# Optimization experiments

Hardware: AMD Instinct MI355X
Metric: run time of the kernel (lower is better)

The kernel has to match this reference:

```python
import jax, jax.numpy as jnp
import numpy as np

B, N = 4, 65536
NUM_GROUP, GROUP_SIZE = 512, 64
EMB = 60


def setup_inputs() -> dict:
    key = jax.random.key(0)
    ks = jax.random.split(key, 8)
    inp = {
        'xyz': jax.random.uniform(ks[0], (B, N, 3), jnp.float32),
        'color': jax.random.uniform(ks[1], (B, N, 3), jnp.float32),
        'W1': jax.random.normal(ks[2], (6, 64), jnp.float32) * 0.2,
        'b1': jnp.zeros((64,), jnp.float32),
        'W2': jax.random.normal(ks[3], (64, 128), jnp.float32) * 0.1,
        'b2': jnp.zeros((128,), jnp.float32),
        'W3': jax.random.normal(ks[4], (128, 256), jnp.float32) * 0.08,
        'b3': jnp.zeros((256,), jnp.float32),
        'W4': jax.random.normal(ks[5], (256, 512), jnp.float32) * 0.06,
        'b4': jnp.zeros((512,), jnp.float32),
        'Wp': jax.random.normal(ks[6], (512, EMB), jnp.float32) * 0.04,
        'bp': jnp.zeros((EMB,), jnp.float32),
    }
    return inp


def fps(xyz, n):
    """Farthest point sampling. xyz: (B,N,3) -> centers (B,n,3)."""
    b, npts, _ = xyz.shape
    start = jnp.zeros((b,), jnp.int32)
    d0 = jnp.full((b, npts), 1e10, xyz.dtype)

    def step(carry, _):
        dists, last = carry
        p = jnp.take_along_axis(xyz, last[:, None, None], axis=1)  # (B,1,3)
        d = jnp.sum((xyz - p) ** 2, axis=-1)                       # (B,N)
        dists = jnp.minimum(dists, d)
        nxt = jnp.argmax(dists, axis=-1).astype(jnp.int32)
        return (dists, nxt), nxt

    (_, _), rest = jax.lax.scan(step, (d0, start), None, length=n - 1)
    idx = jnp.concatenate([start[:, None], rest.T], axis=1)        # (B,n)
    return jax.vmap(lambda pts, i: pts[i])(xyz, idx)


def knn_idx(k, xyz, new_xyz):
    """Indices of k nearest points in xyz for each query in new_xyz.
    xyz: (B,N,3), new_xyz: (B,S,3) -> (B,S,k) int32. Matches
    square_distance + topk(largest=False)."""
    sq = (jnp.sum(new_xyz ** 2, -1)[..., None]
          + jnp.sum(xyz ** 2, -1)[:, None, :]
          - 2.0 * jnp.einsum('bsc,bnc->bsn', new_xyz, xyz))        # (B,S,N)
    _, idx = jax.lax.top_k(-sq, k)
    return idx


def reference(xyz, color, W1, b1, W2, b2, W3, b3, W4, b4, Wp, bp):
    # --- Group: FPS centers + KNN neighborhood gather + centering ---
    center = fps(xyz, NUM_GROUP)                                   # (B,G,3)
    idx = knn_idx(GROUP_SIZE, xyz, center)                         # (B,G,M)
    gather = jax.vmap(lambda pts, i: pts[i])                       # pts[(B,)N,3], i (G,M)
    neighborhood = gather(xyz, idx) - center[:, :, None, :]        # (B,G,M,3) centered
    neighborhood_color = gather(color, idx)                        # (B,G,M,3)
    feats = jnp.concatenate([neighborhood, neighborhood_color], -1)  # (B,G,M,6)

    # --- PointNet: per-point MLP -> max over group -> projection ---
    x = jax.nn.relu(feats @ W1 + b1)
    x = jax.nn.relu(x @ W2 + b2)
    x = jax.nn.relu(x @ W3 + b3)
    x = jax.nn.relu(x @ W4 + b4)                                   # (B,G,M,512)
    x = jnp.max(x, axis=2)                                         # (B,G,512)
    emb = x @ Wp + bp                                              # (B,G,60)
    return emb, center
```

## Files before the change

### kernel.cpp

```cpp
#include <hip/hip_runtime.h>
#include <stdint.h>

#define DI __device__ __forceinline__

typedef _Float16 f16x8 __attribute__((ext_vector_type(8)));
typedef float f32x4 __attribute__((ext_vector_type(4)));
typedef unsigned long long u64;
typedef unsigned short u16;

constexpr int kB = 4;
constexpr int kN = 65536;
constexpr int kG = 512;
constexpr int kM = 64;
constexpr int kE = 60;
constexpr int GRD = 16;
constexpr int NCELL = GRD * GRD * GRD;
constexpr int NSUP = 512;
constexpr float CW = 1.0f / 16.0f;

constexpr int TPB = 512;
constexpr int NWORK = 252;
constexpr int NBLK = 256;

constexpr size_t OFF_CLINE  = 0;
constexpr size_t OFF_CCNT   = OFF_CLINE + (size_t)kB * kG * 128;
constexpr size_t OFF_GS     = OFF_CCNT + (size_t)kB * NCELL * 4;
constexpr size_t ZERO_BYTES = OFF_GS + 64;
constexpr size_t OFF_CSTART = (ZERO_BYTES + 255) & ~(size_t)255;
constexpr size_t OFF_CUR    = OFF_CSTART + (size_t)kB * (NCELL + 1) * 4;
constexpr size_t OFF_DD     = ((OFF_CUR + (size_t)kB * NCELL * 4) + 255) & ~(size_t)255;
constexpr size_t OFF_SW1    = (OFF_DD + (size_t)kB * kN * 4 + 255) & ~(size_t)255;
constexpr size_t OFF_SW2    = OFF_SW1 + 2048 * 2;
constexpr size_t OFF_SW3    = OFF_SW2 + 8192 * 2;
constexpr size_t OFF_SW4    = OFF_SW3 + 32768 * 2;
constexpr size_t OFF_WPT    = OFF_SW4 + 131072 * 2;
constexpr size_t OFF_SORT   = ((OFF_WPT + 60 * 512 * 4) + 255) & ~(size_t)255;

DI int cellof(float x) {
  int c = (int)(x * (float)GRD);
  return min(GRD - 1, max(0, c));
}
DI unsigned orderable(float f) {
  unsigned u = __float_as_uint(f);
  return (u & 0x80000000u) ? ~u : (u | 0x80000000u);
}

__global__ void k_zero(uint32_t* p, int nwords) {
  int i = blockIdx.x * blockDim.x + threadIdx.x;
  int st = gridDim.x * blockDim.x;
  for (; i < nwords; i += st) p[i] = 0u;
}

DI void swz(const float* __restrict__ W, _Float16* __restrict__ sw,
            int total, int nks, int Kreal, int N, int i0, int st) {
  for (int i = i0; i < total; i += st) {
    int j = i & 7, lane = (i >> 3) & 63, rest = i >> 9;
    int ks = rest % nks, nt = rest / nks;
    int k = ks * 32 + ((lane >> 4) << 3) + j;
    int n = nt * 16 + (lane & 15);
    sw[i] = (_Float16)((k < Kreal) ? W[k * N + n] : 0.f);
  }
}

__global__ void k_prep(const float* __restrict__ W1, const float* __restrict__ W2,
                       const float* __restrict__ W3, const float* __restrict__ W4,
                       const float* __restrict__ Wp,
                       _Float16* __restrict__ sw1, _Float16* __restrict__ sw2,
                       _Float16* __restrict__ sw3, _Float16* __restrict__ sw4,
                       float* __restrict__ wpt) {
  int i0 = blockIdx.x * blockDim.x + threadIdx.x;
  int st = gridDim.x * blockDim.x;
  swz(W1, sw1, 2048, 1, 6, 64, i0, st);
  swz(W2, sw2, 8192, 2, 64, 128, i0, st);
  swz(W3, sw3, 32768, 4, 128, 256, i0, st);
  swz(W4, sw4, 131072, 8, 256, 512, i0, st);
  for (int i = i0; i < 60 * 512; i += st) { int n = i >> 9, k = i & 511; wpt[i] = Wp[k * 60 + n]; }
}

DI void gbar(uint32_t* ctr, unsigned target) {
  __syncthreads();
  if (threadIdx.x == 0) {
    __hip_atomic_fetch_add(ctr, 1u, __ATOMIC_ACQ_REL, __HIP_MEMORY_SCOPE_AGENT);
    long bail = 0;
    while (__hip_atomic_load(ctr, __ATOMIC_ACQUIRE, __HIP_MEMORY_SCOPE_AGENT) < target) {
      __builtin_amdgcn_s_sleep(32);
      if (++bail > 100000000L) break;
    }
  }
  __syncthreads();
}

template <bool FIRST>
DI u64 refine_cell(int c, const float4* __restrict__ SP, float* __restrict__ DD,
                   const uint32_t* __restrict__ lcs,
                   float cx, float cy, float cz, int lig) {
  int s0 = (int)lcs[c], s1 = (int)lcs[c + 1];
  int pbase = s0 + lig;
  float4 pt[8];
  float ddo[8];
#pragma unroll
  for (int j = 0; j < 8; ++j) {
    int p = pbase + 4 * j;
    int pc = max(min(p, s1 - 1), 0);
    pt[j] = SP[pc];
    ddo[j] = FIRST ? 1e10f : DD[pc];
  }
  u64 key = 0ull;
#pragma unroll
  for (int j = 0; j < 8; ++j) {
    int p = pbase + 4 * j;
    if (p < s1) {
      float dx = __fsub_rn(pt[j].x, cx);
      float dy = __fsub_rn(pt[j].y, cy);
      float dz = __fsub_rn(pt[j].z, cz);
      float d = __fadd_rn(__fadd_rn(__fmul_rn(dx, dx), __fmul_rn(dy, dy)), __fmul_rn(dz, dz));
      float nd = fminf(ddo[j], d);
      DD[p] = nd;
      u64 k = ((u64)__float_as_uint(nd) << 32) |
              (u64)(0xFFFFFFFFu - (unsigned)__float_as_uint(pt[j].w));
      key = (k > key) ? k : key;
    }
  }
  for (int p = pbase + 32; p < s1; p += 4) {
    float4 pp = SP[p];
    float od = FIRST ? 1e10f : DD[p];
    float dx = __fsub_rn(pp.x, cx);
    float dy = __fsub_rn(pp.y, cy);
    float dz = __fsub_rn(pp.z, cz);
    float d = __fadd_rn(__fadd_rn(__fmul_rn(dx, dx), __fmul_rn(dy, dy)), __fmul_rn(dz, dz));
    float nd = fminf(od, d);
    DD[p] = nd;
    u64 k = ((u64)__float_as_uint(nd) << 32) |
            (u64)(0xFFFFFFFFu - (unsigned)__float_as_uint(pp.w));
    key = (k > key) ? k : key;
  }
  u64 o = __shfl_xor(key, 1); key = (o > key) ? o : key;
  o = __shfl_xor(key, 2); key = (o > key) ? o : key;
  return key;
}

DI void fps_block(const float* __restrict__ xyz, float* __restrict__ outC,
                  u64* __restrict__ cline, uint32_t* __restrict__ gs,
                  const float4* __restrict__ sorted_g,
                  const uint32_t* __restrict__ cstart_g,
                  float* __restrict__ dd_g, int b, char* smem) {
  __builtin_amdgcn_s_setprio(3);
  const int tid = threadIdx.x;
  const int wv = tid >> 6, lane = tid & 63;
  const int grp4 = tid >> 2, lig = tid & 3;
  const float* X = xyz + (size_t)b * kN * 3;
  const float4* SP = sorted_g + (size_t)b * kN;
  float* DD = dd_g + (size_t)b * kN;
  u64* cl = cline + (size_t)b * kG * 16;

  u64* ckey = (u64*)smem;
  uint32_t* lcs = (uint32_t*)(smem + 32768);
  u16* queue = (u16*)(smem + 49408);
  u16* squeue = (u16*)(smem + 57600);
  uint32_t* skey32 = (uint32_t*)(smem + 58624);
  int* qn = (int*)(smem + 60672);
  int* qsn = (int*)(smem + 60676);
  u64* warr = (u64*)(smem + 60736);
  float4* wbuf = (float4*)(smem + 60800);

  float cx = X[0], cy = X[1], cz = X[2];
  if (tid == 0) {
    u64 tg = 1u;
    __hip_atomic_store(cl + 0, ((u64)__float_as_uint(cx) << 32) | tg, __ATOMIC_RELAXED, __HIP_MEMORY_SCOPE_AGENT);
    __hip_atomic_store(cl + 1, ((u64)__float_as_uint(cy) << 32) | tg, __ATOMIC_RELAXED, __HIP_MEMORY_SCOPE_AGENT);
    __hip_atomic_store(cl + 2, ((u64)__float_as_uint(cz) << 32) | tg, __ATOMIC_RELAXED, __HIP_MEMORY_SCOPE_AGENT);
    outC[(size_t)b * kG * 3 + 0] = cx;
    outC[(size_t)b * kG * 3 + 1] = cy;
    outC[(size_t)b * kG * 3 + 2] = cz;
    long bail = 0;
    while (__hip_atomic_load(gs + 2, __ATOMIC_ACQUIRE, __HIP_MEMORY_SCOPE_AGENT) < NWORK) {
      __builtin_amdgcn_s_sleep(16);
      if (++bail > 200000000L) break;
    }
    *qn = 0; *qsn = 0;
  }
  __syncthreads();
  for (int i = tid; i <= NCELL; i += TPB) lcs[i] = cstart_g[(size_t)b * (NCELL + 1) + i];
  __syncthreads();

  for (int it = 1; it < kG; ++it) {
    if (it > 1) {
      {
        int s = tid;
        int sx = s & 7, sy = (s >> 3) & 7, sz = s >> 6;
        float x0 = (float)sx * (2.f * CW);
        float y0 = (float)sy * (2.f * CW);
        float z0 = (float)sz * (2.f * CW);
        float dx = fmaxf(fmaxf(x0 - cx, cx - (x0 + 2.f * CW)), 0.f);
        float dy = fmaxf(fmaxf(y0 - cy, cy - (y0 + 2.f * CW)), 0.f);
        float dz = fmaxf(fmaxf(z0 - cz, cz - (z0 + 2.f * CW)), 0.f);
        float lb = dx * dx + dy * dy + dz * dz;
        bool need = !(lb * 0.999f > __uint_as_float(skey32[s]));
        u64 m = __ballot(need);
        int base = 0;
        if (lane == 0) base = atomicAdd(qsn, (int)__popcll(m));
        base = __shfl(base, 0);
        if (need) squeue[base + (int)__popcll(m & ((1ull << lane) - 1ull))] = (u16)s;
      }
      __syncthreads();
      {
        const int Qs = *qsn;
        int g8 = lane >> 3, lig8 = lane & 7;
        for (int t0 = 0; t0 < Qs; t0 += 64) {
          int t = t0 + wv * 8 + g8;
          bool act = t < Qs;
          int ss = act ? (int)squeue[t] : 0;
          int sx = ss & 7, sy = (ss >> 3) & 7, sz = ss >> 6;
          int cxi = 2 * sx + (lig8 & 1);
          int cyi = 2 * sy + ((lig8 >> 1) & 1);
          int czi = 2 * sz + (lig8 >> 2);
          int c = (czi * GRD + cyi) * GRD + cxi;
          float x0 = (float)cxi * CW, y0 = (float)cyi * CW, z0 = (float)czi * CW;
          float dx = fmaxf(fmaxf(x0 - cx, cx - (x0 + CW)), 0.f);
          float dy = fmaxf(fmaxf(y0 - cy, cy - (y0 + CW)), 0.f);
          float dz = fmaxf(fmaxf(z0 - cz, cz - (z0 + CW)), 0.f);
          float lb = dx * dx + dy * dy + dz * dz;
          float ub = __uint_as_float(((const uint32_t*)ckey)[2 * c + 1]);
          bool need = act && !(lb * 0.999f > ub);
          u64 m = __ballot(need);
          int base = 0;
          if (lane == 0) base = atomicAdd(qn, (int)__popcll(m));
          base = __shfl(base, 0);
          if (need) queue[base + (int)__popcll(m & ((1ull << lane) - 1ull))] = (u16)c;
        }
      }
    }
    __syncthreads();
    if (it == 1) {
      for (int c = grp4; c < NCELL; c += 128) {
        u64 key = refine_cell<true>(c, SP, DD, lcs, cx, cy, cz, lig);
        if (lig == 0) ckey[c] = key;
      }
    } else {
      const int Q = *qn;
      for (int t = grp4; t < Q; t += 128) {
        int c = (int)queue[t];
        u64 key = refine_cell<false>(c, SP, DD, lcs, cx, cy, cz, lig);
        if (lig == 0) ckey[c] = key;
      }
    }
    __syncthreads();
    {
      int s = tid;
      int sx = s & 7, sy = (s >> 3) & 7, sz = s >> 6;
      u64 smax = 0ull;
#pragma unroll
      for (int d = 0; d < 8; ++d) {
        int cxi = 2 * sx + (d & 1);
        int cyi = 2 * sy + ((d >> 1) & 1);
        int czi = 2 * sz + (d >> 2);
        u64 k = ckey[(czi * GRD + cyi) * GRD + cxi];
        smax = (k > smax) ? k : smax;
      }
      skey32[s] = (uint32_t)(smax >> 32);
      u64 key = smax;
#pragma unroll
      for (int off = 32; off; off >>= 1) {
        u64 o = __shfl_xor(key, off);
        key = (o > key) ? o : key;
      }
      if (lane == 0) warr[wv] = key;
    }
    __syncthreads();
    if (tid == 0) {
      u64 k = warr[0];
#pragma unroll
      for (int i = 1; i < 8; ++i) k = (warr[i] > k) ? warr[i] : k;
      unsigned wi = 0xFFFFFFFFu - (unsigned)(k & 0xFFFFFFFFu);
      wbuf[it & 3] = make_float4(X[3 * wi], X[3 * wi + 1], X[3 * wi + 2], 0.f);
      *qn = 0; *qsn = 0;
    }
    __syncthreads();
    float4 wc = wbuf[it & 3];
    cx = wc.x; cy = wc.y; cz = wc.z;
    if ((it & 3) == 3 || it == kG - 1) {
      int k0 = it & ~3;
      if (tid <= (it & 3) && (k0 + tid) >= 1) {
        int itp = k0 + tid;
        float4 w = wbuf[tid];
        u64 tg = (unsigned)(itp + 1);
        u64* e = cl + (size_t)itp * 16;
        __hip_atomic_store(e + 0, ((u64)__float_as_uint(w.x) << 32) | tg, __ATOMIC_RELAXED, __HIP_MEMORY_SCOPE_AGENT);
        __hip_atomic_store(e + 1, ((u64)__float_as_uint(w.y) << 32) | tg, __ATOMIC_RELAXED, __HIP_MEMORY_SCOPE_AGENT);
        __hip_atomic_store(e + 2, ((u64)__float_as_uint(w.z) << 32) | tg, __ATOMIC_RELAXED, __HIP_MEMORY_SCOPE_AGENT);
        outC[((size_t)b * kG + itp) * 3 + 0] = w.x;
        outC[((size_t)b * kG + itp) * 3 + 1] = w.y;
        outC[((size_t)b * kG + itp) * 3 + 2] = w.z;
      }
    }
  }
}

DI void bitonic(u64* a, int n, int tid) {
  for (int k = 2; k <= n; k <<= 1)
    for (int j = k >> 1; j > 0; j >>= 1) {
      __syncthreads();
      for (int i = tid; i < n; i += TPB) {
        int ix = i ^ j;
        if (ix > i) {
          u64 x = a[i], y = a[ix];
          bool up = ((i & k) == 0);
          if ((x > y) == up) { a[i] = y; a[ix] = x; }
        }
      }
    }
  __syncthreads();
}

template <int Kdim, int Ndim, int SIN, int SOUT>
DI void mfma_layer(const _Float16* __restrict__ Xin, _Float16* __restrict__ Xout,
                   const _Float16* __restrict__ Wsw, const float* __restrict__ bias,
                   int wave, int lane) {
  constexpr int NKS = Kdim / 32;
  constexpr int NTW = Ndim / 64;
  constexpr int CH = (NTW < 4) ? NTW : 4;
  const int quad = lane >> 4, l16 = lane & 15;
  for (int c0 = 0; c0 < NTW; c0 += CH) {
    f32x4 acc[CH][4];
#pragma unroll
    for (int nt = 0; nt < CH; ++nt) {
      float bv = bias[wave * (Ndim / 4) + (c0 + nt) * 16 + l16];
#pragma unroll
      for (int m = 0; m < 4; ++m) acc[nt][m] = {bv, bv, bv, bv};
    }
#pragma unroll
    for (int ks = 0; ks < NKS; ++ks) {
      f16x8 af[4];
#pragma unroll
      for (int m = 0; m < 4; ++m)
        af[m] = *(const f16x8*)(Xin + (m * 16 + l16) * SIN + ks * 32 + quad * 8);
#pragma unroll
      for (int nt = 0; nt < CH; ++nt) {
        int ntg = wave * NTW + c0 + nt;
        f16x8 bf = *(const f16x8*)(Wsw + ((size_t)(ntg * NKS + ks) * 64 + lane) * 8);
#pragma unroll
        for (int m = 0; m < 4; ++m)
          acc[nt][m] = __builtin_amdgcn_mfma_f32_16x16x32_f16(af[m], bf, acc[nt][m], 0, 0, 0);
      }
    }
#pragma unroll
    for (int nt = 0; nt < CH; ++nt) {
      int col = wave * (Ndim / 4) + (c0 + nt) * 16 + l16;
#pragma unroll
      for (int m = 0; m < 4; ++m)
#pragma unroll
        for (int r = 0; r < 4; ++r) {
          int row = m * 16 + quad * 4 + r;
          Xout[row * SOUT + col] = (_Float16)fmaxf(acc[nt][m][r], 0.f);
        }
    }
  }
}

DI void mfma_layer4(const _Float16* __restrict__ Xin, const _Float16* __restrict__ Wsw,
                    const float* __restrict__ bias, float* __restrict__ maxv,
                    int wave, int lane) {
  constexpr int SIN = 264, NKS = 8, NTW = 8, CH = 4;
  const int quad = lane >> 4, l16 = lane & 15;
  for (int c0 = 0; c0 < NTW; c0 += CH) {
    f32x4 acc[CH][4];
#pragma unroll
    for (int nt = 0; nt < CH; ++nt) {
      float bv = bias[wave * 128 + (c0 + nt) * 16 + l16];
#pragma unroll
      for (int m = 0; m < 4; ++m) acc[nt][m] = {bv, bv, bv, bv};
    }
#pragma unroll
    for (int ks = 0; ks < NKS; ++ks) {
      f16x8 af[4];
#pragma unroll
      for (int m = 0; m < 4; ++m)
        af[m] = *(const f16x8*)(Xin + (m * 16 + l16) * SIN + ks * 32 + quad * 8);
#pragma unroll
      for (int nt = 0; nt < CH; ++nt) {
        int ntg = wave * NTW + c0 + nt;
        f16x8 bf = *(const f16x8*)(Wsw + ((size_t)(ntg * NKS + ks) * 64 + lane) * 8);
#pragma unroll
        for (int m = 0; m < 4; ++m)
          acc[nt][m] = __builtin_amdgcn_mfma_f32_16x16x32_f16(af[m], bf, acc[nt][m], 0, 0, 0);
      }
    }
#pragma unroll
    for (int nt = 0; nt < CH; ++nt) {
      float mx = 0.f;
#pragma unroll
      for (int m = 0; m < 4; ++m)
#pragma unroll
        for (int r = 0; r < 4; ++r) mx = fmaxf(mx, acc[nt][m][r]);
      mx = fmaxf(mx, __shfl_xor(mx, 16, 64));
      mx = fmaxf(mx, __shfl_xor(mx, 32, 64));
      if (quad == 0) maxv[wave * 128 + (c0 + nt) * 16 + l16] = mx;
    }
  }
}

__global__ __launch_bounds__(TPB, 2) void k_fused(
    const float* __restrict__ xyz, const float* __restrict__ color,
    float* __restrict__ outC, float* __restrict__ outE,
    u64* __restrict__ cline, uint32_t* __restrict__ ccnt,
    uint32_t* __restrict__ cstart, uint32_t* __restrict__ cur,
    float4* __restrict__ sorted, float* __restrict__ dd_g,
    uint32_t* __restrict__ gs,
    const _Float16* __restrict__ sw1, const _Float16* __restrict__ sw2,
    const _Float16* __restrict__ sw3, const _Float16* __restrict__ sw4,
    const float* __restrict__ wpt,
    const float* __restrict__ b1, const float* __restrict__ b2,
    const float* __restrict__ b3, const float* __restrict__ b4,
    const float* __restrict__ bp) {
  __shared__ __align__(16) char smem[65536];
  const int bi = blockIdx.x;
  if (bi < kB) {
    fps_block(xyz, outC, cline, gs, sorted, cstart, dd_g, bi, smem);
    return;
  }

  const int wj = bi - kB;
  const int tid = threadIdx.x;
  const int wave = tid >> 6, lane = tid & 63;
  __shared__ int nC;
  __shared__ float4 spc;
  __shared__ uint32_t s_part[TPB];
  u64* cand = (u64*)smem;

  for (int i = wj * TPB + tid; i < kB * kN; i += NWORK * TPB) {
    int b = i >> 16, p = i & (kN - 1);
    const float* q = xyz + ((size_t)b * kN + p) * 3;
    int cid = (cellof(q[2]) * GRD + cellof(q[1])) * GRD + cellof(q[0]);
    atomicAdd(&ccnt[b * NCELL + cid], 1u);
  }
  gbar(gs + 0, NWORK);
  if (wj < kB) {
    int b = wj;
    const uint32_t* cc = ccnt + (size_t)b * NCELL;
    uint32_t* cs = cstart + (size_t)b * (NCELL + 1);
    uint32_t* cu = cur + (size_t)b * NCELL;
    const int chunk = NCELL / TPB;
    int c0 = tid * chunk;
    uint32_t s = 0;
    for (int i = 0; i < chunk; ++i) s += cc[c0 + i];
    s_part[tid] = s;
    __syncthreads();
    for (int off = 1; off < TPB; off <<= 1) {
      uint32_t add = (tid >= off) ? s_part[tid - off] : 0u;
      __syncthreads();
      s_part[tid] += add;
      __syncthreads();
    }
    uint32_t run = s_part[tid] - s;
    for (int i = 0; i < chunk; ++i) {
      int c = c0 + i;
      cs[c] = run; cu[c] = run; run += cc[c];
    }
    if (tid == TPB - 1) cs[NCELL] = run;
  }
  gbar(gs + 1, NWORK);
  for (int i = wj * TPB + tid; i < kB * kN; i += NWORK * TPB) {
    int b = i >> 16, p = i & (kN - 1);
    const float* q = xyz + ((size_t)b * kN + p) * 3;
    float x = q[0], y = q[1], z = q[2];
    int cid = (cellof(z) * GRD + cellof(y)) * GRD + cellof(x);
    uint32_t pos = atomicAdd(&cur[b * NCELL + cid], 1u);
    sorted[(size_t)b * kN + pos] = make_float4(x, y, z, __uint_as_float((unsigned)p));
  }
  gbar(gs + 2, NWORK);

  for (int j = wj; j < kB * kG; j += NWORK) {
    const int it = j >> 2, b = j & 3;
    if (tid < 64) {
      const u64* e = cline + ((size_t)b * kG + it) * 16;
      u64 v = 0; long bail = 0;
      for (;;) {
        if (lane < 3)
          v = __hip_atomic_load(e + lane, __ATOMIC_RELAXED, __HIP_MEMORY_SCOPE_AGENT);
        bool ok = (lane >= 3) || ((unsigned)v == (unsigned)(it + 1));
        if (__all(ok)) break;
        __builtin_amdgcn_s_sleep(8);
        if (++bail > 100000000L) break;
      }
      u64 v0 = __shfl(v, 0), v1 = __shfl(v, 1), v2 = __shfl(v, 2);
      if (tid == 0)
        spc = make_float4(__uint_as_float((unsigned)(v0 >> 32)),
                          __uint_as_float((unsigned)(v1 >> 32)),
                          __uint_as_float((unsigned)(v2 >> 32)), 0.f);
    }
    __syncthreads();
    const float cx = spc.x, cy = spc.y, cz = spc.z;

    const float nc = __fadd_rn(__fadd_rn(__fmul_rn(cx, cx), __fmul_rn(cy, cy)), __fmul_rn(cz, cz));
    const float4* SPb = sorted + (size_t)b * kN;
    const uint32_t* CS = cstart + (size_t)b * (NCELL + 1);
    const int ccx = cellof(cx), ccy = cellof(cy), ccz = cellof(cz);
    if (tid == 0) nC = 0;
    __syncthreads();
    int plox = 1, phix = 0, ploy = 1, phiy = 0, ploz = 1, phiz = 0;
    for (int r = 1; r <= GRD; ++r) {
      int lox = max(0, ccx - r), hix = min(GRD - 1, ccx + r);
      int loy = max(0, ccy - r), hiy = min(GRD - 1, ccy + r);
      int loz = max(0, ccz - r), hiz = min(GRD - 1, ccz + r);
      for (int z = loz; z <= hiz; ++z)
        for (int y = loy; y <= hiy; ++y) {
          bool rowPrev = (r > 1) && (z >= ploz && z <= phiz && y >= ploy && y <= phiy);
          for (int s = 0; s < 2; ++s) {
            int xa, xb;
            if (!rowPrev) { if (s) break; xa = lox; xb = hix; }
            else if (s == 0) { xa = lox; xb = plox - 1; }
            else { xa = phix + 1; xb = hix; }
            if (xa > xb) continue;
            int c0 = (z * GRD + y) * GRD + xa;
            int i0 = CS[c0];
            int i1 = CS[(z * GRD + y) * GRD + xb + 1];
            for (int i = i0 + tid; i < i1; i += TPB) {
              float4 pt = SPb[i];
              float npn = __fadd_rn(__fadd_rn(__fmul_rn(pt.x, pt.x), __fmul_rn(pt.y, pt.y)),
                                    __fmul_rn(pt.z, pt.z));
              float dot = __fadd_rn(__fadd_rn(__fmul_rn(cx, pt.x), __fmul_rn(cy, pt.y)),
                                    __fmul_rn(cz, pt.z));
              float sq = __fsub_rn(__fadd_rn(nc, npn), __fmul_rn(2.0f, dot));
              unsigned key = orderable(sq);
              int pos = atomicAdd(&nC, 1);
              if (pos < 8192)
                cand[pos] = ((u64)key << 32) | (unsigned)__float_as_uint(pt.w);
            }
          }
        }
      __syncthreads();
      int n = min(nC, 8192);
      float rc = 1e30f;
      if (lox > 0) rc = fminf(rc, cx - (float)lox * CW);
      if (hix < GRD - 1) rc = fminf(rc, (float)(hix + 1) * CW - cx);
      if (loy > 0) rc = fminf(rc, cy - (float)loy * CW);
      if (hiy < GRD - 1) rc = fminf(rc, (float)(hiy + 1) * CW - cy);
      if (loz > 0) rc = fminf(rc, cz - (float)loz * CW);
      if (hiz < GRD - 1) rc = fminf(rc, (float)(hiz + 1) * CW - cz);
      float r2 = (rc >= 1e29f) ? 3.0e38f : rc * rc * (1.0f - 1e-5f);
      unsigned keyR = orderable(r2);
      bool done = false;
      if (n >= kM) {
        int np2 = 1;
        while (np2 < n) np2 <<= 1;
        for (int i = n + tid; i < np2; i += TPB) cand[i] = ~0ull;
        bitonic(cand, np2, tid);
        unsigned k63 = (unsigned)(cand[kM - 1] >> 32);
        done = (k63 <= keyR);
        if (tid == 0) nC = n;
      }
      __syncthreads();
      if (done) break;
      plox = lox; phix = hix; ploy = loy; phiy = hiy; ploz = loz; phiz = hiz;
    }

    uint32_t pidx = 0;
    if (tid < kM) pidx = (uint32_t)(cand[tid] & 0xFFFFFFFFu);
    __syncthreads();
    _Float16* bufA = (_Float16*)smem;
    _Float16* bufB = (_Float16*)(smem + 17408);
    float* maxv = (float*)smem;
    float* psum = (float*)(smem + 2048);
    if (tid < kM) {
      const float* xp = xyz + ((size_t)b * kN + pidx) * 3;
      const float* cp = color + ((size_t)b * kN + pidx) * 3;
      f16x8 v = {};
      v[0] = (_Float16)__fsub_rn(xp[0], cx);
      v[1] = (_Float16)__fsub_rn(xp[1], cy);
      v[2] = (_Float16)__fsub_rn(xp[2], cz);
      v[3] = (_Float16)cp[0];
      v[4] = (_Float16)cp[1];
      v[5] = (_Float16)cp[2];
      f16x8 zf = {};
      *(f16x8*)(bufA + tid * 40 + 0) = v;
      *(f16x8*)(bufA + tid * 40 + 8) = zf;
      *(f16x8*)(bufA + tid * 40 + 16) = zf;
      *(f16x8*)(bufA + tid * 40 + 24) = zf;
    }
    __syncthreads();
    if (tid < 256) mfma_layer<32, 64, 40, 72>(bufA, bufB, sw1, b1, wave, lane);
    __syncthreads();
    if (tid < 256) mfma_layer<64, 128, 72, 136>(bufB, bufA, sw2, b2, wave, lane);
    __syncthreads();
    if (tid < 256) mfma_layer<128, 256, 136, 264>(bufA, bufB, sw3, b3, wave, lane);
    __syncthreads();
    if (tid < 256) mfma_layer4(bufB, sw4, b4, maxv, wave, lane);
    __syncthreads();
    if (tid < 240) {
      int jj = tid >> 2, q = tid & 3;
      const float* w = wpt + (size_t)jj * 512 + q * 128;
      float s = 0.f;
#pragma unroll 4
      for (int k = 0; k < 128; ++k) s = fmaf(maxv[q * 128 + k], w[k], s);
      psum[tid] = s;
    }
    __syncthreads();
    if (tid < kE) {
      float e = __fadd_rn(__fadd_rn(psum[tid * 4 + 0], psum[tid * 4 + 1]),
                          __fadd_rn(psum[tid * 4 + 2], psum[tid * 4 + 3])) + bp[tid];
      outE[((size_t)b * kG + it) * kE + tid] = e;
    }
    __syncthreads();
  }
}

extern "C" void kernel_launch(void* const* d_in, const int* in_sizes, int n_in,
                              void* d_out, int out_size, void* d_ws, size_t ws_size,
                              hipStream_t stream) {
  (void)in_sizes; (void)n_in; (void)out_size; (void)ws_size;
  const float* xyz = (const float*)d_in[0];
  const float* color = (const float*)d_in[1];
  const float* W1 = (const float*)d_in[2];
  const float* b1 = (const float*)d_in[3];
  const float* W2 = (const float*)d_in[4];
  const float* b2 = (const float*)d_in[5];
  const float* W3 = (const float*)d_in[6];
  const float* b3 = (const float*)d_in[7];
  const float* W4 = (const float*)d_in[8];
  const float* b4 = (const float*)d_in[9];
  const float* Wp = (const float*)d_in[10];
  const float* bp = (const float*)d_in[11];

  char* ws = (char*)d_ws;
  auto cline = (u64*)(ws + OFF_CLINE);
  auto ccnt = (uint32_t*)(ws + OFF_CCNT);
  auto gs = (uint32_t*)(ws + OFF_GS);
  auto cstart = (uint32_t*)(ws + OFF_CSTART);
  auto cur = (uint32_t*)(ws + OFF_CUR);
  auto dd = (float*)(ws + OFF_DD);
  auto sw1 = (_Float16*)(ws + OFF_SW1);
  auto sw2 = (_Float16*)(ws + OFF_SW2);
  auto sw3 = (_Float16*)(ws + OFF_SW3);
  auto sw4 = (_Float16*)(ws + OFF_SW4);
  auto wpt = (float*)(ws + OFF_WPT);
  auto sorted = (float4*)(ws + OFF_SORT);

  float* outE = (float*)d_out;
  float* outC = outE + (size_t)kB * kG * kE;

  k_zero<<<256, 256, 0, stream>>>((uint32_t*)ws, (int)(ZERO_BYTES / 4));
  k_prep<<<256, 256, 0, stream>>>(W1, W2, W3, W4, Wp, sw1, sw2, sw3, sw4, wpt);
  k_fused<<<NBLK, TPB, 0, stream>>>(xyz, color, outC, outE, cline, ccnt, cstart,
                                    cur, sorted, dd, gs, sw1, sw2, sw3, sw4, wpt,
                                    b1, b2, b3, b4, bp);
}
```

Before: 2.010 ms.

## Replace shared work queues in FPS with static per-group cell ownership

Removes the two-level supercell/cell queue construction, with its atomics and extra barriers, from each FPS iteration. Each 4-thread group now statically owns 32 strided cells, tests their bounds itself, merges the need mask across the group with shuffles, and refines the needed cells two at a time so loads from both cells are in flight together. This cuts per-iteration barriers and LDS atomics on the serial FPS critical path. The cost is possible load imbalance, since busy cells are no longer spread evenly across all groups.

```diff
diff --git a/kernel.cpp b/kernel.cpp
--- a/kernel.cpp
+++ b/kernel.cpp
@@ -15,7 +15,6 @@
 constexpr int kE = 60;
 constexpr int GRD = 16;
 constexpr int NCELL = GRD * GRD * GRD;
-constexpr int NSUP = 512;
 constexpr float CW = 1.0f / 16.0f;
 
 constexpr int TPB = 512;
@@ -90,40 +89,52 @@
   __syncthreads();
 }
 
-template <bool FIRST>
-DI u64 refine_cell(int c, const float4* __restrict__ SP, float* __restrict__ DD,
-                   const uint32_t* __restrict__ lcs,
-                   float cx, float cy, float cz, int lig) {
-  int s0 = (int)lcs[c], s1 = (int)lcs[c + 1];
-  int pbase = s0 + lig;
-  float4 pt[8];
-  float ddo[8];
+DI void refine_pair(int c0, int c1, const float4* __restrict__ SP,
+                    float* __restrict__ DD, const uint32_t* __restrict__ lcs,
+                    float cx, float cy, float cz, int lig, bool first,
+                    u64* __restrict__ ckey) {
+  const int a0 = (int)lcs[c0], a1 = (int)lcs[c0 + 1];
+  const int baseA = a0 + lig;
+  float4 pA[8]; float dA[8];
 #pragma unroll
   for (int j = 0; j < 8; ++j) {
-    int p = pbase + 4 * j;
-    int pc = max(min(p, s1 - 1), 0);
-    pt[j] = SP[pc];
-    ddo[j] = FIRST ? 1e10f : DD[pc];
-  }
-  u64 key = 0ull;
+    int p = baseA + 4 * j;
+    int pc = max(min(p, a1 - 1), 0);
+    pA[j] = SP[pc];
+    dA[j] = first ? 1e10f : DD[pc];
+  }
+  int b0 = 0, b1 = 0, baseB = 0;
+  float4 pB[8]; float dB[8];
+  if (c1 >= 0) {
+    b0 = (int)lcs[c1]; b1 = (int)lcs[c1 + 1];
+    baseB = b0 + lig;
+#pragma unroll
+    for (int j = 0; j < 8; ++j) {
+      int p = baseB + 4 * j;
+      int pc = max(min(p, b1 - 1), 0);
+      pB[j] = SP[pc];
+      dB[j] = first ? 1e10f : DD[pc];
+    }
+  }
+  u64 keyA = 0ull;
 #pragma unroll
   for (int j = 0; j < 8; ++j) {
-    int p = pbase + 4 * j;
-    if (p < s1) {
-      float dx = __fsub_rn(pt[j].x, cx);
-      float dy = __fsub_rn(pt[j].y, cy);
-      float dz = __fsub_rn(pt[j].z, cz);
+    int p = baseA + 4 * j;
+    if (p < a1) {
+      float dx = __fsub_rn(pA[j].x, cx);
+      float dy = __fsub_rn(pA[j].y, cy);
+      float dz = __fsub_rn(pA[j].z, cz);
       float d = __fadd_rn(__fadd_rn(__fmul_rn(dx, dx), __fmul_rn(dy, dy)), __fmul_rn(dz, dz));
-      float nd = fminf(ddo[j], d);
+      float nd = fminf(dA[j], d);
       DD[p] = nd;
       u64 k = ((u64)__float_as_uint(nd) << 32) |
-              (u64)(0xFFFFFFFFu - (unsigned)__float_as_uint(pt[j].w));
-      key = (k > key) ? k : key;
-    }
-  }
-  for (int p = pbase + 32; p < s1; p += 4) {
+              (u64)(0xFFFFFFFFu - (unsigned)__float_as_uint(pA[j].w));
+      keyA = (k > keyA) ? k : keyA;
+    }
+  }
+  for (int p = baseA + 32; p < a1; p += 4) {
     float4 pp = SP[p];
-    float od = FIRST ? 1e10f : DD[p];
+    float od = first ? 1e10f : DD[p];
     float dx = __fsub_rn(pp.x, cx);
     float dy = __fsub_rn(pp.y, cy);
     float dz = __fsub_rn(pp.z, cz);
@@ -132,11 +143,45 @@
     DD[p] = nd;
     u64 k = ((u64)__float_as_uint(nd) << 32) |
             (u64)(0xFFFFFFFFu - (unsigned)__float_as_uint(pp.w));
-    key = (k > key) ? k : key;
-  }
-  u64 o = __shfl_xor(key, 1); key = (o > key) ? o : key;
-  o = __shfl_xor(key, 2); key = (o > key) ? o : key;
-  return key;
+    keyA = (k > keyA) ? k : keyA;
+  }
+  u64 o = __shfl_xor(keyA, 1); keyA = (o > keyA) ? o : keyA;
+  o = __shfl_xor(keyA, 2); keyA = (o > keyA) ? o : keyA;
+  if (lig == 0) ckey[c0] = keyA;
+  if (c1 >= 0) {
+    u64 keyB = 0ull;
+#pragma unroll
+    for (int j = 0; j < 8; ++j) {
+      int p = baseB + 4 * j;
+      if (p < b1) {
+        float dx = __fsub_rn(pB[j].x, cx);
+        float dy = __fsub_rn(pB[j].y, cy);
+        float dz = __fsub_rn(pB[j].z, cz);
+        float d = __fadd_rn(__fadd_rn(__fmul_rn(dx, dx), __fmul_rn(dy, dy)), __fmul_rn(dz, dz));
+        float nd = fminf(dB[j], d);
+        DD[p] = nd;
+        u64 k = ((u64)__float_as_uint(nd) << 32) |
+                (u64)(0xFFFFFFFFu - (unsigned)__float_as_uint(pB[j].w));
+        keyB = (k > keyB) ? k : keyB;
+      }
+    }
+    for (int p = baseB + 32; p < b1; p += 4) {
+      float4 pp = SP[p];
+      float od = first ? 1e10f : DD[p];
+      float dx = __fsub_rn(pp.x, cx);
+      float dy = __fsub_rn(pp.y, cy);
+      float dz = __fsub_rn(pp.z, cz);
+      float d = __fadd_rn(__fadd_rn(__fmul_rn(dx, dx), __fmul_rn(dy, dy)), __fmul_rn(dz, dz));
+      float nd = fminf(od, d);
+      DD[p] = nd;
+      u64 k = ((u64)__float_as_uint(nd) << 32) |
+              (u64)(0xFFFFFFFFu - (unsigned)__float_as_uint(pp.w));
+      keyB = (k > keyB) ? k : keyB;
+    }
+    o = __shfl_xor(keyB, 1); keyB = (o > keyB) ? o : keyB;
+    o = __shfl_xor(keyB, 2); keyB = (o > keyB) ? o : keyB;
+    if (lig == 0) ckey[c1] = keyB;
+  }
 }
 
 DI void fps_block(const float* __restrict__ xyz, float* __restrict__ outC,
@@ -147,7 +192,8 @@
   __builtin_amdgcn_s_setprio(3);
   const int tid = threadIdx.x;
   const int wv = tid >> 6, lane = tid & 63;
-  const int grp4 = tid >> 2, lig = tid & 3;
+  const int grp = tid >> 2, lig = tid & 3;
+  const int gx = grp & 3, gy = (grp >> 2) & 3, gz = grp >> 4;
   const float* X = xyz + (size_t)b * kN * 3;
   const float4* SP = sorted_g + (size_t)b * kN;
   float* DD = dd_g + (size_t)b * kN;
@@ -155,13 +201,8 @@
 
   u64* ckey = (u64*)smem;
   uint32_t* lcs = (uint32_t*)(smem + 32768);
-  u16* queue = (u16*)(smem + 49408);
-  u16* squeue = (u16*)(smem + 57600);
-  uint32_t* skey32 = (uint32_t*)(smem + 58624);
-  int* qn = (int*)(smem + 60672);
-  int* qsn = (int*)(smem + 60676);
-  u64* warr = (u64*)(smem + 60736);
-  float4* wbuf = (float4*)(smem + 60800);
+  u64* warr = (u64*)(smem + 49408);
+  float4* wbuf = (float4*)(smem + 49472);
 
   float cx = X[0], cy = X[1], cz = X[2];
   if (tid == 0) {
@@ -177,95 +218,63 @@
       __builtin_amdgcn_s_sleep(16);
       if (++bail > 200000000L) break;
     }
-    *qn = 0; *qsn = 0;
   }
   __syncthreads();
   for (int i = tid; i <= NCELL; i += TPB) lcs[i] = cstart_g[(size_t)b * (NCELL + 1) + i];
   __syncthreads();
 
   for (int it = 1; it < kG; ++it) {
-    if (it > 1) {
-      {
-        int s = tid;
-        int sx = s & 7, sy = (s >> 3) & 7, sz = s >> 6;
-        float x0 = (float)sx * (2.f * CW);
-        float y0 = (float)sy * (2.f * CW);
-        float z0 = (float)sz * (2.f * CW);
-        float dx = fmaxf(fmaxf(x0 - cx, cx - (x0 + 2.f * CW)), 0.f);
-        float dy = fmaxf(fmaxf(y0 - cy, cy - (y0 + 2.f * CW)), 0.f);
-        float dz = fmaxf(fmaxf(z0 - cz, cz - (z0 + 2.f * CW)), 0.f);
+    const bool first = (it == 1);
+    unsigned mask;
+    if (first) {
+      mask = 0xFFFFFFFFu;
+    } else {
+      unsigned pm = 0;
+#pragma unroll
+      for (int j = 0; j < 8; ++j) {
+        int m = lig * 8 + j;
+        int cxi = gx + 4 * (m & 3);
+        int cyi = gy + 4 * ((m >> 2) & 3);
+        int czi = gz + 8 * (m >> 4);
+        int c = (czi * GRD + cyi) * GRD + cxi;
+        float x0 = (float)cxi * CW;
+        float y0 = (float)cyi * CW;
+        float z0 = (float)czi * CW;
+        float dx = fmaxf(fmaxf(x0 - cx, cx - (x0 + CW)), 0.f);
+        float dy = fmaxf(fmaxf(y0 - cy, cy - (y0 + CW)), 0.f);
+        float dz = fmaxf(fmaxf(z0 - cz, cz - (z0 + CW)), 0.f);
         float lb = dx * dx + dy * dy + dz * dz;
-        bool need = !(lb * 0.999f > __uint_as_float(skey32[s]));
-        u64 m = __ballot(need);
-        int base = 0;
-        if (lane == 0) base = atomicAdd(qsn, (int)__popcll(m));
-        base = __shfl(base, 0);
-        if (need) squeue[base + (int)__popcll(m & ((1ull << lane) - 1ull))] = (u16)s;
-      }
-      __syncthreads();
-      {
-        const int Qs = *qsn;
-        int g8 = lane >> 3, lig8 = lane & 7;
-        for (int t0 = 0; t0 < Qs; t0 += 64) {
-          int t = t0 + wv * 8 + g8;
-          bool act = t < Qs;
-          int ss = act ? (int)squeue[t] : 0;
-          int sx = ss & 7, sy = (ss >> 3) & 7, sz = ss >> 6;
-          int cxi = 2 * sx + (lig8 & 1);
-          int cyi = 2 * sy + ((lig8 >> 1) & 1);
-          int czi = 2 * sz + (lig8 >> 2);
-          int c = (czi * GRD + cyi) * GRD + cxi;
-          float x0 = (float)cxi * CW, y0 = (float)cyi * CW, z0 = (float)czi * CW;
-          float dx = fmaxf(fmaxf(x0 - cx, cx - (x0 + CW)), 0.f);
-          float dy = fmaxf(fmaxf(y0 - cy, cy - (y0 + CW)), 0.f);
-          float dz = fmaxf(fmaxf(z0 - cz, cz - (z0 + CW)), 0.f);
-          float lb = dx * dx + dy * dy + dz * dz;
-          float ub = __uint_as_float(((const uint32_t*)ckey)[2 * c + 1]);
-          bool need = act && !(lb * 0.999f > ub);
-          u64 m = __ballot(need);
-          int base = 0;
-          if (lane == 0) base = atomicAdd(qn, (int)__popcll(m));
-          base = __shfl(base, 0);
-          if (need) queue[base + (int)__popcll(m & ((1ull << lane) - 1ull))] = (u16)c;
-        }
-      }
-    }
-    __syncthreads();
-    if (it == 1) {
-      for (int c = grp4; c < NCELL; c += 128) {
-        u64 key = refine_cell<true>(c, SP, DD, lcs, cx, cy, cz, lig);
-        if (lig == 0) ckey[c] = key;
-      }
-    } else {
-      const int Q = *qn;
-      for (int t = grp4; t < Q; t += 128) {
-        int c = (int)queue[t];
-        u64 key = refine_cell<false>(c, SP, DD, lcs, cx, cy, cz, lig);
-        if (lig == 0) ckey[c] = key;
-      }
-    }
-    __syncthreads();
-    {
-      int s = tid;
-      int sx = s & 7, sy = (s >> 3) & 7, sz = s >> 6;
-      u64 smax = 0ull;
-#pragma unroll
-      for (int d = 0; d < 8; ++d) {
-        int cxi = 2 * sx + (d & 1);
-        int cyi = 2 * sy + ((d >> 1) & 1);
-        int czi = 2 * sz + (d >> 2);
-        u64 k = ckey[(czi * GRD + cyi) * GRD + cxi];
-        smax = (k > smax) ? k : smax;
-      }
-      skey32[s] = (uint32_t)(smax >> 32);
-      u64 key = smax;
-#pragma unroll
-      for (int off = 32; off; off >>= 1) {
-        u64 o = __shfl_xor(key, off);
-        key = (o > key) ? o : key;
-      }
-      if (lane == 0) warr[wv] = key;
-    }
+        float ub = __uint_as_float(((const uint32_t*)ckey)[2 * c + 1]);
+        if (!(lb * 0.999f > ub)) pm |= 1u << m;
+      }
+      pm |= __shfl_xor(pm, 1);
+      pm |= __shfl_xor(pm, 2);
+      mask = pm;
+    }
+    while (mask) {
+      int m0 = __ffs(mask) - 1; mask &= mask - 1;
+      int m1 = -1;
+      if (mask) { m1 = __ffs(mask) - 1; mask &= mask - 1; }
+      int c0 = ((gz + 8 * (m0 >> 4)) * GRD + (gy + 4 * ((m0 >> 2) & 3))) * GRD + (gx + 4 * (m0 & 3));
+      int c1 = (m1 >= 0)
+             ? ((gz + 8 * (m1 >> 4)) * GRD + (gy + 4 * ((m1 >> 2) & 3))) * GRD + (gx + 4 * (m1 & 3))
+             : -1;
+      refine_pair(c0, c1, SP, DD, lcs, cx, cy, cz, lig, first, ckey);
+    }
+    u64 gkey = 0ull;
+#pragma unroll
+    for (int j = 0; j < 8; ++j) {
+      int m = lig * 8 + j;
+      int c = ((gz + 8 * (m >> 4)) * GRD + (gy + 4 * ((m >> 2) & 3))) * GRD + (gx + 4 * (m & 3));
+      u64 k = ckey[c];
+      gkey = (k > gkey) ? k : gkey;
+    }
+#pragma unroll
+    for (int off = 1; off < 64; off <<= 1) {
+      u64 o = __shfl_xor(gkey, off);
+      gkey = (o > gkey) ? o : gkey;
+    }
+    if (lane == 0) warr[wv] = gkey;
     __syncthreads();
     if (tid == 0) {
       u64 k = warr[0];
@@ -273,7 +282,6 @@
       for (int i = 1; i < 8; ++i) k = (warr[i] > k) ? warr[i] : k;
       unsigned wi = 0xFFFFFFFFu - (unsigned)(k & 0xFFFFFFFFu);
       wbuf[it & 3] = make_float4(X[3 * wi], X[3 * wi + 1], X[3 * wi + 2], 0.f);
-      *qn = 0; *qsn = 0;
     }
     __syncthreads();
     float4 wc = wbuf[it & 3];
```

Measured after the change: 2.247 ms. +11.8%, slower.
